# Performance work log

Measured on AMD Instinct MI355X. Metric: run time of the kernel, lower is better.

The kernel has to match this reference:

```python
import jax, jax.numpy as jnp
import numpy as np

D_MODEL = 1024
N_HEADS = 16
D_FF = 4096
EPS = 1e-6


def layernorm(x, alpha, bias):
    # torch.std uses Bessel correction (ddof=1)
    mean = jnp.mean(x, axis=-1, keepdims=True)
    std = jnp.std(x, axis=-1, keepdims=True, ddof=1)
    return alpha * (x - mean) / (std + EPS) + bias


def setup_inputs() -> dict:
    key = jax.random.key(0)
    ks = jax.random.split(key, 12)
    s = 1.0 / np.sqrt(D_MODEL)
    sf = 1.0 / np.sqrt(D_FF)
    return {
        "x": jax.random.normal(ks[0], (2, 2048, D_MODEL), jnp.float32),
        "mask": jnp.ones((2, 1, 1, 2048), jnp.int32),
        "wq": jax.random.normal(ks[1], (D_MODEL, D_MODEL), jnp.float32) * s,
        "wk": jax.random.normal(ks[2], (D_MODEL, D_MODEL), jnp.float32) * s,
        "wv": jax.random.normal(ks[3], (D_MODEL, D_MODEL), jnp.float32) * s,
        "wo": jax.random.normal(ks[4], (D_MODEL, D_MODEL), jnp.float32) * s,
        "wo_b": jnp.zeros((D_MODEL,), jnp.float32),
        "w1": jax.random.normal(ks[5], (D_MODEL, D_FF), jnp.float32) * s,
        "b1": jnp.zeros((D_FF,), jnp.float32),
        "w2": jax.random.normal(ks[6], (D_FF, D_MODEL), jnp.float32) * sf,
        "b2": jnp.zeros((D_MODEL,), jnp.float32),
        "alpha1": jnp.ones((D_MODEL,), jnp.float32),
        "bias1": jnp.zeros((D_MODEL,), jnp.float32),
        "alpha2": jnp.ones((D_MODEL,), jnp.float32),
        "bias2": jnp.zeros((D_MODEL,), jnp.float32),
    }


def reference(x, mask, wq, wk, wv, wo, wo_b, w1, b1, w2, b2,
              alpha1, bias1, alpha2, bias2):
    B, S, D = x.shape
    h, dk = N_HEADS, D_MODEL // N_HEADS
    # projections -> [B, h, S, dk]
    q = (x @ wq).reshape(B, S, h, dk).transpose(0, 2, 1, 3)
    k = (x @ wk).reshape(B, S, h, dk).transpose(0, 2, 1, 3)
    v = (x @ wv).reshape(B, S, h, dk).transpose(0, 2, 1, 3)
    scores = jnp.einsum('bhqd,bhkd->bhqk', q, k) / jnp.sqrt(jnp.float32(dk))
    scores = jnp.where(mask == 0, jnp.float32(-1e9), scores)
    attn = jax.nn.softmax(scores, axis=-1)
    ctx = jnp.einsum('bhqk,bhkd->bhqd', attn, v)
    ctx = ctx.transpose(0, 2, 1, 3).reshape(B, S, D)
    attn_out = ctx @ wo + wo_b
    x = layernorm(x + attn_out, alpha1, bias1)
    ff = jax.nn.relu(x @ w1 + b1) @ w2 + b2
    x = layernorm(x + ff, alpha2, bias2)
    return x
```

## Files before the change

### kernel.cpp

```cpp
#include <hip/hip_runtime.h>
#include <hip/hip_bf16.h>

#define D_MODEL 1024
#define N_HEADS 16
#define DK      64
#define SEQ     2048
#define BATCH   2
#define D_FF    4096
#define ROWS    (BATCH*SEQ)
#define LN_EPS  1e-6f
#define KTILE   128

typedef __hip_bfloat16 bf16;
typedef __attribute__((ext_vector_type(8))) short frag8;
typedef __attribute__((ext_vector_type(4))) float facc4;

__device__ inline float bf2f(unsigned short u){ return __uint_as_float(((unsigned)u) << 16); }
__device__ inline float toF(bf16 v){ return __bfloat162float(v); }
__device__ inline unsigned short f2bu(float f){ bf16 h = __float2bfloat16(f); return *reinterpret_cast<unsigned short*>(&h); }

__device__ inline unsigned cvtpk_bf16(float lo, float hi){
    unsigned r;
    asm("v_cvt_pk_bf16_f32 %0, %1, %2" : "=v"(r) : "v"(lo), "v"(hi));
    return r;
}

__device__ inline float ld1(const void* p, size_t idx, bool f32) {
    return f32 ? ((const float*)p)[idx] : toF(((const bf16*)p)[idx]);
}

struct U8 { unsigned short v[8]; };
__device__ inline U8 ld8bf(const void* p, size_t idx, bool f32) {
    U8 r;
    if (!f32) {
        *reinterpret_cast<uint4*>(r.v) = *reinterpret_cast<const uint4*>((const unsigned short*)p + idx);
    } else {
        const float* f = (const float*)p + idx;
        const float4 a = *reinterpret_cast<const float4*>(f);
        const float4 b = *reinterpret_cast<const float4*>(f + 4);
        r.v[0]=f2bu(a.x); r.v[1]=f2bu(a.y); r.v[2]=f2bu(a.z); r.v[3]=f2bu(a.w);
        r.v[4]=f2bu(b.x); r.v[5]=f2bu(b.y); r.v[6]=f2bu(b.z); r.v[7]=f2bu(b.w);
    }
    return r;
}

__device__ inline void gld16(const void* g, void* l) {
    __builtin_amdgcn_global_load_lds(
        reinterpret_cast<const __attribute__((address_space(1))) void*>(
            reinterpret_cast<uintptr_t>(g)),
        reinterpret_cast<__attribute__((address_space(3))) void*>(
            (unsigned int)reinterpret_cast<uintptr_t>(l)),
        16, 0, 0);
}

__global__ void probe_kernel(const void* __restrict__ xp, int* __restrict__ flag) {
    __shared__ int hit;
    if (threadIdx.x == 0) hit = 0;
    __syncthreads();
    const bf16* p = (const bf16*)xp;
    int bad = 0;
    for (int i = threadIdx.x; i < 8192; i += 256) {
        float v = fabsf(toF(p[i]));
        if (!(v <= 1e5f)) bad = 1;
    }
    if (bad) atomicOr(&hit, 1);
    __syncthreads();
    if (threadIdx.x == 0) *flag = hit;
}

__global__ __launch_bounds__(256) void xcvt_kernel(const void* __restrict__ x,
    bf16* __restrict__ out, const int* __restrict__ flagp)
{
    const bool f32 = (*flagp) != 0;
    const size_t i = ((size_t)blockIdx.x * 256 + threadIdx.x) * 8;
    U8 d = ld8bf(x, i, f32);
    *reinterpret_cast<uint4*>(out + i) = *reinterpret_cast<const uint4*>(d.v);
}

__global__ __launch_bounds__(256) void transpose_kernel(const void* __restrict__ W,
    bf16* __restrict__ WT, int K, int N, const int* __restrict__ flagp)
{
    const bool f32 = (*flagp) != 0;
    __shared__ float tile[64][65];
    const int t  = threadIdx.x;
    const int n0 = blockIdx.x * 64, k0 = blockIdx.y * 64;
    const int lr = t >> 2;
    const int lc = (t & 3) * 16;
    if (!f32) {
        const unsigned short* src = (const unsigned short*)W + (size_t)(k0 + lr) * N + n0 + lc;
        uint4 u0 = *reinterpret_cast<const uint4*>(src);
        uint4 u1 = *reinterpret_cast<const uint4*>(src + 8);
        const unsigned short* us0 = reinterpret_cast<const unsigned short*>(&u0);
        const unsigned short* us1 = reinterpret_cast<const unsigned short*>(&u1);
        #pragma unroll
        for (int j = 0; j < 8; ++j) {
            tile[lr][lc + j]     = bf2f(us0[j]);
            tile[lr][lc + 8 + j] = bf2f(us1[j]);
        }
    } else {
        const float* src = (const float*)W + (size_t)(k0 + lr) * N + n0 + lc;
        #pragma unroll
        for (int q4 = 0; q4 < 4; ++q4) {
            const float4 f = *reinterpret_cast<const float4*>(src + 4 * q4);
            tile[lr][lc + 4*q4 + 0] = f.x;
            tile[lr][lc + 4*q4 + 1] = f.y;
            tile[lr][lc + 4*q4 + 2] = f.z;
            tile[lr][lc + 4*q4 + 3] = f.w;
        }
    }
    __syncthreads();
    unsigned short o[16];
    #pragma unroll
    for (int j = 0; j < 16; ++j) o[j] = f2bu(tile[lc + j][lr]);
    bf16* dst = WT + (size_t)(n0 + lr) * K + k0 + lc;
    *reinterpret_cast<uint4*>(dst)     = *reinterpret_cast<const uint4*>(&o[0]);
    *reinterpret_cast<uint4*>(dst + 8) = *reinterpret_cast<const uint4*>(&o[8]);
}

__global__ __launch_bounds__(256) void transpose4_kernel(const void* __restrict__ w0,
    const void* __restrict__ w1, const void* __restrict__ w2, const void* __restrict__ w3,
    bf16* __restrict__ WT4, const int* __restrict__ flagp)
{
    const bool f32 = (*flagp) != 0;
    const int which = blockIdx.z;
    const void* W = (which == 0) ? w0 : (which == 1) ? w1 : (which == 2) ? w2 : w3;
    bf16* WT = WT4 + (size_t)which * D_MODEL * D_MODEL;
    __shared__ float tile[64][65];
    const int t  = threadIdx.x;
    const int n0 = blockIdx.x * 64, k0 = blockIdx.y * 64;
    const int lr = t >> 2;
    const int lc = (t & 3) * 16;
    if (!f32) {
        const unsigned short* src = (const unsigned short*)W + (size_t)(k0 + lr) * D_MODEL + n0 + lc;
        uint4 u0 = *reinterpret_cast<const uint4*>(src);
        uint4 u1 = *reinterpret_cast<const uint4*>(src + 8);
        const unsigned short* us0 = reinterpret_cast<const unsigned short*>(&u0);
        const unsigned short* us1 = reinterpret_cast<const unsigned short*>(&u1);
        #pragma unroll
        for (int j = 0; j < 8; ++j) {
            tile[lr][lc + j]     = bf2f(us0[j]);
            tile[lr][lc + 8 + j] = bf2f(us1[j]);
        }
    } else {
        const float* src = (const float*)W + (size_t)(k0 + lr) * D_MODEL + n0 + lc;
        #pragma unroll
        for (int q4 = 0; q4 < 4; ++q4) {
            const float4 f = *reinterpret_cast<const float4*>(src + 4 * q4);
            tile[lr][lc + 4*q4 + 0] = f.x;
            tile[lr][lc + 4*q4 + 1] = f.y;
            tile[lr][lc + 4*q4 + 2] = f.z;
            tile[lr][lc + 4*q4 + 3] = f.w;
        }
    }
    __syncthreads();
    unsigned short o[16];
    #pragma unroll
    for (int j = 0; j < 16; ++j) o[j] = f2bu(tile[lc + j][lr]);
    bf16* dst = WT + (size_t)(n0 + lr) * D_MODEL + k0 + lc;
    *reinterpret_cast<uint4*>(dst)     = *reinterpret_cast<const uint4*>(&o[0]);
    *reinterpret_cast<uint4*>(dst + 8) = *reinterpret_cast<const uint4*>(&o[8]);
}

__global__ __launch_bounds__(256) void vtrans_kernel(const bf16* __restrict__ V,
    bf16* __restrict__ VT)
{
    __shared__ unsigned short tile[32][33];
    const int tx = threadIdx.x, ty = threadIdx.y;
    const int s0 = blockIdx.x * 32, d0 = blockIdx.y * 32;
    const int bh = blockIdx.z, b = bh >> 4, h = bh & 15;
    #pragma unroll
    for (int r = 0; r < 4; ++r)
        tile[ty + 8*r][tx] = *reinterpret_cast<const unsigned short*>(
            V + ((size_t)(b * SEQ + s0 + ty + 8*r)) * D_MODEL + h * DK + d0 + tx);
    __syncthreads();
    #pragma unroll
    for (int r = 0; r < 4; ++r)
        *reinterpret_cast<unsigned short*>(
            VT + ((size_t)(bh * DK + d0 + ty + 8*r)) * SEQ + s0 + tx) = tile[tx][ty + 8*r];
}

template<bool RELU, bool BIAS, int NMAT, int SPLITK>
__global__ __launch_bounds__(256) void mgemm_kernel(const bf16* __restrict__ A,
    const bf16* __restrict__ BT, const void* __restrict__ bias,
    bf16* __restrict__ C, int M, int N, int K, const int* __restrict__ flagp)
{
    const bool inF32 = (*flagp) != 0;

    __shared__ unsigned short sA[128 * 64];
    __shared__ unsigned short sB[128 * 64];

    int which = 0, colb = blockIdx.x;
    if (NMAT > 1) { which = blockIdx.x >> 3; colb = blockIdx.x & 7; }
    const int kslice = (SPLITK > 1) ? blockIdx.z : 0;
    const int Kspan  = K / SPLITK;
    const int kbase  = kslice * Kspan;
    const bf16* Bp = BT + (size_t)which * N * K;
    bf16*       Cp = C  + (size_t)which * M * N + (size_t)kslice * M * N;

    const int row0 = blockIdx.y * 128;
    const int col0 = colb * 128;

    const int t    = threadIdx.x;
    const int wave = t >> 6;
    const int lane = t & 63;
    const int lm   = lane & 15;
    const int q    = lane >> 4;
    const int wm   = (wave & 1) * 64;
    const int wn   = (wave >> 1) * 64;

    facc4 acc[4][4];
    #pragma unroll
    for (int i = 0; i < 4; ++i)
        #pragma unroll
        for (int j = 0; j < 4; ++j)
            acc[i][j] = (facc4){0.f, 0.f, 0.f, 0.f};

    for (int k0 = kbase; k0 < kbase + Kspan; k0 += 64) {
        __syncthreads();
        #pragma unroll
        for (int j = 0; j < 4; ++j) {
            const int ch = (wave * 4 + j) * 64 + lane;
            const int r  = ch >> 3;
            const int cs = ch & 7;
            const int c  = cs ^ (r & 7);
            gld16(A  + (size_t)(row0 + r) * K + k0 + 8 * c, &sA[(wave * 4 + j) * 512]);
            gld16(Bp + (size_t)(col0 + r) * K + k0 + 8 * c, &sB[(wave * 4 + j) * 512]);
        }
        __syncthreads();

        #pragma unroll
        for (int kk = 0; kk < 64; kk += 32) {
            const int cr = (kk >> 3) + q;
            frag8 af[4], bfr[4];
            #pragma unroll
            for (int im = 0; im < 4; ++im) {
                const int m = wm + 16 * im + lm;
                af[im] = *reinterpret_cast<const frag8*>(&sA[m * 64 + ((cr ^ (m & 7)) << 3)]);
            }
            #pragma unroll
            for (int in = 0; in < 4; ++in) {
                const int n = wn + 16 * in + lm;
                bfr[in] = *reinterpret_cast<const frag8*>(&sB[n * 64 + ((cr ^ (n & 7)) << 3)]);
            }
            #pragma unroll
            for (int im = 0; im < 4; ++im)
                #pragma unroll
                for (int in = 0; in < 4; ++in)
                    acc[im][in] = __builtin_amdgcn_mfma_f32_16x16x32_bf16(af[im], bfr[in], acc[im][in], 0, 0, 0);
        }
    }

    #pragma unroll
    for (int in = 0; in < 4; ++in) {
        const int col = col0 + wn + 16*in + lm;
        float bv = 0.f;
        if (BIAS && kslice == 0) bv = ld1(bias, col, inF32);
        #pragma unroll
        for (int im = 0; im < 4; ++im) {
            #pragma unroll
            for (int r = 0; r < 4; ++r) {
                const int row = row0 + wm + 16*im + 4*q + r;
                float v = acc[im][in][r] + bv;
                if (RELU) v = fmaxf(v, 0.f);
                Cp[(size_t)row * N + col] = __float2bfloat16(v);
            }
        }
    }
}

__global__ __launch_bounds__(256, 2) void fattn_kernel(
    const bf16* __restrict__ Qg, const bf16* __restrict__ Kg,
    const bf16* __restrict__ VTg, const int* __restrict__ mask,
    bf16* __restrict__ ctx)
{
    __shared__ unsigned short sK[2][128 * 64];
    __shared__ unsigned short sV[2][64 * 128];
    __shared__ __align__(16) float madd[SEQ];

    const int t    = threadIdx.x;
    const int lin  = blockIdx.x + 16 * (blockIdx.y + 16 * blockIdx.z);
    const int rid  = (lin & 7) * 64 + (lin >> 3);
    const int qt   = rid & 15;
    const int h    = (rid >> 4) & 15;
    const int b    = rid >> 8;
    const int q0   = qt * 128;
    const int bh   = b * N_HEADS + h;
    const int wave = t >> 6;
    const int lane = t & 63;
    const int lm   = lane & 15;
    const int qd   = lane >> 4;
    const bool qo  = (qd & 1) != 0;

    const float SCL = 0.18033688011112042f;

    auto stage = [&](int bi, int kt) {
        const int k0 = kt * KTILE;
        #pragma unroll
        for (int j = 0; j < 4; ++j) {
            const int ch = (wave * 4 + j) * 64 + lane;
            const int rK = ch >> 3, cK = (ch & 7) ^ (rK & 7);
            gld16(Kg + ((size_t)(b * SEQ + k0 + rK)) * D_MODEL + h * DK + 8 * cK,
                  &sK[bi][(wave * 4 + j) * 512]);
            const int rV = ch >> 4, cV = (ch & 15) ^ (rV & 15);
            gld16(VTg + ((size_t)(bh * DK + rV)) * SEQ + k0 + 8 * cV,
                  &sV[bi][(wave * 4 + j) * 512]);
        }
    };

    stage(0, 0);
    #pragma unroll
    for (int i = 0; i < SEQ / 256; ++i) {
        const int idx = i * 256 + t;
        madd[idx] = (mask[b * SEQ + idx] == 0) ? -1.442695e9f : 0.f;
    }

    frag8 qf[2][2];
    #pragma unroll
    for (int s = 0; s < 2; ++s) {
        const bf16* qsrc = Qg + ((size_t)(b * SEQ + q0 + 32 * wave + 16 * s + lm)) * D_MODEL + h * DK;
        qf[s][0] = *reinterpret_cast<const frag8*>(qsrc + 8 * qd);
        qf[s][1] = *reinterpret_cast<const frag8*>(qsrc + 32 + 8 * qd);
    }

    facc4 accO[2][4];
    #pragma unroll
    for (int s = 0; s < 2; ++s)
        #pragma unroll
        for (int in = 0; in < 4; ++in) accO[s][in] = (facc4){0.f, 0.f, 0.f, 0.f};
    float m_r[2] = {-1e30f, -1e30f}, l_r[2] = {0.f, 0.f};

    for (int kt = 0; kt < SEQ / KTILE; ++kt) {
        const int cur = kt & 1;
        const int k0  = kt * KTILE;
        __syncthreads();
        if (kt + 1 < SEQ / KTILE) stage(cur ^ 1, kt + 1);

        facc4 accST[2][8];
        #pragma unroll
        for (int s = 0; s < 2; ++s)
            #pragma unroll
            for (int i = 0; i < 8; ++i) accST[s][i] = (facc4){0.f, 0.f, 0.f, 0.f};
        __builtin_amdgcn_s_setprio(1);
        #pragma unroll
        for (int i = 0; i < 8; ++i) {
            #pragma unroll
            for (int s2 = 0; s2 < 2; ++s2) {
                const int cr = 4 * s2 + qd;
                frag8 kf = *reinterpret_cast<const frag8*>(
                    &sK[cur][(16 * i + lm) * 64 + ((cr ^ (lm & 7)) << 3)]);
                accST[0][i] = __builtin_amdgcn_mfma_f32_16x16x32_bf16(kf, qf[0][s2], accST[0][i], 0, 0, 0);
                accST[1][i] = __builtin_amdgcn_mfma_f32_16x16x32_bf16(kf, qf[1][s2], accST[1][i], 0, 0, 0);
            }
        }
        __builtin_amdgcn_s_setprio(0);

        facc4 vmx[2];
        #pragma unroll
        for (int s = 0; s < 2; ++s) vmx[s] = (facc4){-1e30f, -1e30f, -1e30f, -1e30f};
        #pragma unroll
        for (int i = 0; i < 8; ++i) {
            const facc4 mv = *reinterpret_cast<const facc4*>(&madd[k0 + 16 * i + 4 * qd]);
            #pragma unroll
            for (int s = 0; s < 2; ++s) {
                #pragma unroll
                for (int r = 0; r < 4; ++r) {
                    accST[s][i][r] = fmaf(accST[s][i][r], SCL, mv[r]);
                    vmx[s][r] = fmaxf(vmx[s][r], accST[s][i][r]);
                }
            }
        }
        float mn[2], alpha[2] = {1.f, 1.f};
        bool resc[2];
        #pragma unroll
        for (int s = 0; s < 2; ++s) {
            const float mloc = fmaxf(fmaxf(vmx[s][0], vmx[s][1]), fmaxf(vmx[s][2], vmx[s][3]));
            const bool skip = __all(mloc - m_r[s] <= 11.54f) != 0;
            resc[s] = !skip;
            if (skip) {
                mn[s] = m_r[s];
            } else {
                float m0 = mloc;
                m0 = fmaxf(m0, __shfl_xor(m0, 16));
                m0 = fmaxf(m0, __shfl_xor(m0, 32));
                mn[s] = fmaxf(m_r[s], m0);
                alpha[s] = __builtin_amdgcn_exp2f(m_r[s] - mn[s]);
                m_r[s] = mn[s];
            }
        }

        unsigned up[2][8][2];
        facc4 ps4[2];
        #pragma unroll
        for (int s = 0; s < 2; ++s) ps4[s] = (facc4){0.f, 0.f, 0.f, 0.f};
        #pragma unroll
        for (int s = 0; s < 2; ++s) {
            #pragma unroll
            for (int i = 0; i < 8; ++i) {
                const float p0 = __builtin_amdgcn_exp2f(accST[s][i][0] - mn[s]);
                const float p1 = __builtin_amdgcn_exp2f(accST[s][i][1] - mn[s]);
                const float p2 = __builtin_amdgcn_exp2f(accST[s][i][2] - mn[s]);
                const float p3 = __builtin_amdgcn_exp2f(accST[s][i][3] - mn[s]);
                ps4[s][0] += p0; ps4[s][1] += p1; ps4[s][2] += p2; ps4[s][3] += p3;
                up[s][i][0] = cvtpk_bf16(p0, p1);
                up[s][i][1] = cvtpk_bf16(p2, p3);
            }
        }
        #pragma unroll
        for (int s = 0; s < 2; ++s) {
            float ps = (ps4[s][0] + ps4[s][1]) + (ps4[s][2] + ps4[s][3]);
            ps += __shfl_xor(ps, 16);
            ps += __shfl_xor(ps, 32);
            if (resc[s]) {
                l_r[s] = l_r[s] * alpha[s] + ps;
                #pragma unroll
                for (int in = 0; in < 4; ++in)
                    #pragma unroll
                    for (int r = 0; r < 4; ++r) accO[s][in][r] *= alpha[s];
            } else {
                l_r[s] += ps;
            }
        }

        __builtin_amdgcn_s_setprio(1);
        #pragma unroll
        for (int c = 0; c < 4; ++c) {
            union { frag8 f; unsigned u[4]; } pf0_, pf1_;
            #pragma unroll
            for (int s = 0; s < 2; ++s) {
                unsigned a0 = up[s][2*c][0],     a1 = up[s][2*c][1];
                unsigned b0 = up[s][2*c + 1][0], b1 = up[s][2*c + 1][1];
                asm("v_permlane32_swap_b32 %0, %1" : "+v"(a0), "+v"(b0));
                asm("v_permlane32_swap_b32 %0, %1" : "+v"(a1), "+v"(b1));
                const unsigned t0 = qo ? a0 : b0;
                const unsigned t1 = qo ? a1 : b1;
                const unsigned r0 = __shfl_xor(t0, 16);
                const unsigned r1 = __shfl_xor(t1, 16);
                unsigned u0 = qo ? r0 : a0;
                unsigned u1 = qo ? r1 : a1;
                unsigned u2 = qo ? b0 : r0;
                unsigned u3 = qo ? b1 : r1;
                if (s == 0) { pf0_.u[0]=u0; pf0_.u[1]=u1; pf0_.u[2]=u2; pf0_.u[3]=u3; }
                else        { pf1_.u[0]=u0; pf1_.u[1]=u1; pf1_.u[2]=u2; pf1_.u[3]=u3; }
            }
            #pragma unroll
            for (int in = 0; in < 4; ++in) {
                const int cr = 4 * c + qd;
                frag8 vf = *reinterpret_cast<const frag8*>(
                    &sV[cur][(16 * in + lm) * 128 + ((cr ^ lm) << 3)]);
                accO[0][in] = __builtin_amdgcn_mfma_f32_16x16x32_bf16(vf, pf0_.f, accO[0][in], 0, 0, 0);
                accO[1][in] = __builtin_amdgcn_mfma_f32_16x16x32_bf16(vf, pf1_.f, accO[1][in], 0, 0, 0);
            }
        }
        __builtin_amdgcn_s_setprio(0);
    }

    #pragma unroll
    for (int s = 0; s < 2; ++s) {
        const float invl = 1.f / l_r[s];
        bf16* crow = ctx + ((size_t)(b * SEQ + q0 + 32 * wave + 16 * s + lm)) * D_MODEL + h * DK;
        #pragma unroll
        for (int in = 0; in < 4; ++in) {
            union { uint2 v; unsigned u[2]; } ov;
            ov.u[0] = cvtpk_bf16(accO[s][in][0] * invl, accO[s][in][1] * invl);
            ov.u[1] = cvtpk_bf16(accO[s][in][2] * invl, accO[s][in][3] * invl);
            *reinterpret_cast<uint2*>(crow + 16 * in + 4 * qd) = ov.v;
        }
    }
}

template<bool BASE_WS, bool OUT_WS>
__global__ __launch_bounds__(128) void ln_kernel(const void* __restrict__ base,
    const bf16* __restrict__ addv, const bf16* __restrict__ addv2,
    const void* __restrict__ alpha, const void* __restrict__ bias,
    void* __restrict__ outp, const int* __restrict__ flagp)
{
    const bool inF32 = (*flagp) != 0;
    __shared__ float red[2];
    __shared__ float red2[2];
    const int row = blockIdx.x, t = threadIdx.x;
    const size_t off = (size_t)row * D_MODEL + t * 8;

    float v[8];
    {
        const U8 bz = ld8bf(base, off, BASE_WS ? false : inF32);
        uint4 a1 = *reinterpret_cast<const uint4*>(addv + off);
        const unsigned short* a1s = reinterpret_cast<const unsigned short*>(&a1);
        #pragma unroll
        for (int j = 0; j < 8; ++j) v[j] = bf2f(bz.v[j]) + bf2f(a1s[j]);
        if (addv2) {
            uint4 a2 = *reinterpret_cast<const uint4*>(addv2 + off);
            const unsigned short* a2s = reinterpret_cast<const unsigned short*>(&a2);
            #pragma unroll
            for (int j = 0; j < 8; ++j) v[j] += bf2f(a2s[j]);
        }
    }

    float s = ((v[0]+v[1]) + (v[2]+v[3])) + ((v[4]+v[5]) + (v[6]+v[7]));
    #pragma unroll
    for (int o = 1; o < 64; o <<= 1) s += __shfl_xor(s, o);
    if ((t & 63) == 0) red[t >> 6] = s;
    __syncthreads();
    const float mean = (red[0] + red[1]) * (1.f / (float)D_MODEL);

    float sq = 0.f;
    #pragma unroll
    for (int j = 0; j < 8; ++j) { const float d = v[j] - mean; sq += d * d; }
    #pragma unroll
    for (int o = 1; o < 64; o <<= 1) sq += __shfl_xor(sq, o);
    if ((t & 63) == 0) red2[t >> 6] = sq;
    __syncthreads();
    const float var = (red2[0] + red2[1]) * (1.f / (float)(D_MODEL - 1));
    const float inv = 1.f / (sqrtf(var) + LN_EPS);

    float y[8];
    #pragma unroll
    for (int j = 0; j < 8; ++j)
        y[j] = ld1(alpha, t * 8 + j, inF32) * (v[j] - mean) * inv + ld1(bias, t * 8 + j, inF32);

    if (OUT_WS || !inF32) {
        union { uint4 u; unsigned w[4]; } o_;
        o_.w[0] = cvtpk_bf16(y[0], y[1]);
        o_.w[1] = cvtpk_bf16(y[2], y[3]);
        o_.w[2] = cvtpk_bf16(y[4], y[5]);
        o_.w[3] = cvtpk_bf16(y[6], y[7]);
        *reinterpret_cast<uint4*>((bf16*)outp + off) = o_.u;
    } else {
        float* op = (float*)outp + off;
        const float4 f0 = {y[0], y[1], y[2], y[3]};
        const float4 f1 = {y[4], y[5], y[6], y[7]};
        *reinterpret_cast<float4*>(op)     = f0;
        *reinterpret_cast<float4*>(op + 4) = f1;
    }
}

extern "C" void kernel_launch(void* const* d_in, const int* in_sizes, int n_in,
                              void* d_out, int out_size, void* d_ws, size_t ws_size,
                              hipStream_t stream)
{
    const void* x    = d_in[0];
    const int*  mask = (const int*)d_in[1];
    const void* wq   = d_in[2];
    const void* wk   = d_in[3];
    const void* wv   = d_in[4];
    const void* wo   = d_in[5];
    const void* wo_b = d_in[6];
    const void* w1   = d_in[7];
    const void* b1   = d_in[8];
    const void* w2   = d_in[9];
    const void* b2   = d_in[10];
    const void* al1  = d_in[11];
    const void* bi1  = d_in[12];
    const void* al2  = d_in[13];
    const void* bi2  = d_in[14];

    const size_t MB = 1024 * 1024;
    char* ws = (char*)d_ws;
    const bool BIG = ws_size >= 64 * MB + 4096;
    if (!BIG && ws_size < 56 * MB + 4096) return;

    dim3 tb(32, 8);

    if (BIG) {
        bf16* Qb   = (bf16*)(ws + 0 * MB);
        bf16* Kb   = (bf16*)(ws + 8 * MB);
        bf16* Vb   = (bf16*)(ws + 16 * MB);
        bf16* Xb   = (bf16*)(ws + 24 * MB);
        bf16* VTb  = (bf16*)(ws + 24 * MB);
        bf16* WT4  = (bf16*)(ws + 32 * MB);
        bf16* WOT  = WT4 + (size_t)3 * D_MODEL * D_MODEL;
        bf16* W1T  = (bf16*)(ws + 40 * MB);
        bf16* W2T  = (bf16*)(ws + 48 * MB);
        bf16* CTXb = (bf16*)(ws + 56 * MB);
        bf16* ATT0 = (bf16*)(ws + 0 * MB);
        bf16* ATT1 = (bf16*)(ws + 8 * MB);
        bf16* X1b  = (bf16*)(ws + 56 * MB);
        bf16* FFb  = (bf16*)(ws + 0 * MB);
        bf16* X20  = (bf16*)(ws + 32 * MB);
        bf16* X21  = (bf16*)(ws + 40 * MB);
        int*  flagp = (int*)(ws + 64 * MB);

        probe_kernel<<<1, 256, 0, stream>>>(x, flagp);
        xcvt_kernel<<<dim3(ROWS * D_MODEL / 2048), 256, 0, stream>>>(x, Xb, flagp);

        transpose4_kernel<<<dim3(16, 16, 4), 256, 0, stream>>>(wq, wk, wv, wo, WT4, flagp);
        transpose_kernel<<<dim3(64, 16), 256, 0, stream>>>(w1, W1T, D_MODEL, D_FF, flagp);
        transpose_kernel<<<dim3(16, 64), 256, 0, stream>>>(w2, W2T, D_FF, D_MODEL, flagp);

        mgemm_kernel<false, false, 3, 1><<<dim3(24, 32), 256, 0, stream>>>(
            Xb, WT4, nullptr, Qb, ROWS, D_MODEL, D_MODEL, flagp);

        vtrans_kernel<<<dim3(SEQ / 32, 2, BATCH * N_HEADS), tb, 0, stream>>>(Vb, VTb);

        fattn_kernel<<<dim3(SEQ / 128, N_HEADS, BATCH), 256, 0, stream>>>(Qb, Kb, VTb, mask, CTXb);

        mgemm_kernel<false, true, 1, 2><<<dim3(8, 32, 2), 256, 0, stream>>>(
            CTXb, WOT, wo_b, ATT0, ROWS, D_MODEL, D_MODEL, flagp);
        ln_kernel<false, true><<<ROWS, 128, 0, stream>>>(x, ATT0, ATT1, al1, bi1, X1b, flagp);

        mgemm_kernel<true, true, 1, 1><<<dim3(32, 32), 256, 0, stream>>>(
            X1b, W1T, b1, FFb, ROWS, D_FF, D_MODEL, flagp);

        mgemm_kernel<false, true, 1, 2><<<dim3(8, 32, 2), 256, 0, stream>>>(
            FFb, W2T, b2, X20, ROWS, D_MODEL, D_FF, flagp);
        ln_kernel<true, false><<<ROWS, 128, 0, stream>>>(X1b, X20, X21, al2, bi2, d_out, flagp);
    } else {
        bf16* Qb    = (bf16*)(ws + 0 * MB);
        bf16* Kb    = (bf16*)(ws + 8 * MB);
        bf16* Vb    = (bf16*)(ws + 16 * MB);
        bf16* Xb    = (bf16*)(ws + 24 * MB);
        bf16* VTb   = (bf16*)(ws + 24 * MB);
        bf16* WQKVT = (bf16*)(ws + 32 * MB);
        bf16* CTXb  = (bf16*)(ws + 32 * MB);
        bf16* W2T   = (bf16*)(ws + 32 * MB);
        bf16* WOT   = (bf16*)(ws + 0 * MB);
        bf16* ATT0  = (bf16*)(ws + 48 * MB);
        bf16* W1T   = (bf16*)(ws + 48 * MB);
        bf16* X20   = (bf16*)(ws + 48 * MB);
        bf16* X1b   = (bf16*)(ws + 40 * MB);
        bf16* FFb   = (bf16*)(ws + 0 * MB);
        int*  flagp = (int*)(ws + 56 * MB);

        probe_kernel<<<1, 256, 0, stream>>>(x, flagp);
        xcvt_kernel<<<dim3(ROWS * D_MODEL / 2048), 256, 0, stream>>>(x, Xb, flagp);

        transpose_kernel<<<dim3(16, 16), 256, 0, stream>>>(wq, WQKVT,           D_MODEL, D_MODEL, flagp);
        transpose_kernel<<<dim3(16, 16), 256, 0, stream>>>(wk, WQKVT + 1048576, D_MODEL, D_MODEL, flagp);
        transpose_kernel<<<dim3(16, 16), 256, 0, stream>>>(wv, WQKVT + 2097152, D_MODEL, D_MODEL, flagp);

        mgemm_kernel<false, false, 3, 1><<<dim3(24, 32), 256, 0, stream>>>(
            Xb, WQKVT, nullptr, Qb, ROWS, D_MODEL, D_MODEL, flagp);

        vtrans_kernel<<<dim3(SEQ / 32, 2, BATCH * N_HEADS), tb, 0, stream>>>(Vb, VTb);

        fattn_kernel<<<dim3(SEQ / 128, N_HEADS, BATCH), 256, 0, stream>>>(Qb, Kb, VTb, mask, CTXb);

        transpose_kernel<<<dim3(16, 16), 256, 0, stream>>>(wo, WOT, D_MODEL, D_MODEL, flagp);
        mgemm_kernel<false, true, 1, 1><<<dim3(8, 32), 256, 0, stream>>>(
            CTXb, WOT, wo_b, ATT0, ROWS, D_MODEL, D_MODEL, flagp);
        ln_kernel<false, true><<<ROWS, 128, 0, stream>>>(x, ATT0, nullptr, al1, bi1, X1b, flagp);

        transpose_kernel<<<dim3(64, 16), 256, 0, stream>>>(w1, W1T, D_MODEL, D_FF, flagp);
        mgemm_kernel<true, true, 1, 1><<<dim3(32, 32), 256, 0, stream>>>(
            X1b, W1T, b1, FFb, ROWS, D_FF, D_MODEL, flagp);

        transpose_kernel<<<dim3(16, 64), 256, 0, stream>>>(w2, W2T, D_FF, D_MODEL, flagp);
        mgemm_kernel<false, true, 1, 1><<<dim3(8, 32), 256, 0, stream>>>(
            FFb, W2T, b2, X20, ROWS, D_MODEL, D_FF, flagp);
        ln_kernel<true, false><<<ROWS, 128, 0, stream>>>(X1b, X20, nullptr, al2, bi2, d_out, flagp);
    }
}
```

Measured before the change: 381.4 us.

## Fuse V transpose into QKV GEMM epilogue and merge FF weight transposes

The QKV GEMM now writes the V projection directly in per-head transposed layout [b,h,d,s], which removes the separate vtrans kernel and its extra read and write of V. The two FFN weight transposes are merged into one launch. The attention mask is loaded as int4 vectors, and layernorm loads alpha and bias as 8-wide vectors. The transposed V epilogue uses strided 8-byte stores that may coalesce less well than the normal row-major epilogue.

```diff
diff --git a/kernel.cpp b/kernel.cpp
--- a/kernel.cpp
+++ b/kernel.cpp
@@ -44,6 +44,21 @@
     return r;
 }
 
+__device__ inline void ld8f(const void* p, int idx, bool f32, float* o) {
+    if (!f32) {
+        uint4 u = *reinterpret_cast<const uint4*>((const unsigned short*)p + idx);
+        const unsigned short* us = reinterpret_cast<const unsigned short*>(&u);
+        #pragma unroll
+        for (int j = 0; j < 8; ++j) o[j] = bf2f(us[j]);
+    } else {
+        const float* f = (const float*)p + idx;
+        const float4 a = *reinterpret_cast<const float4*>(f);
+        const float4 b = *reinterpret_cast<const float4*>(f + 4);
+        o[0]=a.x; o[1]=a.y; o[2]=a.z; o[3]=a.w;
+        o[4]=b.x; o[5]=b.y; o[6]=b.z; o[7]=b.w;
+    }
+}
+
 __device__ inline void gld16(const void* g, void* l) {
     __builtin_amdgcn_global_load_lds(
         reinterpret_cast<const __attribute__((address_space(1))) void*>(
@@ -77,13 +92,9 @@
     *reinterpret_cast<uint4*>(out + i) = *reinterpret_cast<const uint4*>(d.v);
 }
 
-__global__ __launch_bounds__(256) void transpose_kernel(const void* __restrict__ W,
-    bf16* __restrict__ WT, int K, int N, const int* __restrict__ flagp)
-{
-    const bool f32 = (*flagp) != 0;
-    __shared__ float tile[64][65];
-    const int t  = threadIdx.x;
-    const int n0 = blockIdx.x * 64, k0 = blockIdx.y * 64;
+__device__ inline void ttile(const void* W, bf16* WT, int K, int N,
+                             int n0, int k0, bool f32, float (*tile)[65], int t)
+{
     const int lr = t >> 2;
     const int lc = (t & 3) * 16;
     if (!f32) {
@@ -117,66 +128,37 @@
     *reinterpret_cast<uint4*>(dst + 8) = *reinterpret_cast<const uint4*>(&o[8]);
 }
 
+__global__ __launch_bounds__(256) void transpose_kernel(const void* __restrict__ W,
+    bf16* __restrict__ WT, int K, int N, const int* __restrict__ flagp)
+{
+    __shared__ float tile[64][65];
+    ttile(W, WT, K, N, blockIdx.x * 64, blockIdx.y * 64, (*flagp) != 0, tile, threadIdx.x);
+}
+
 __global__ __launch_bounds__(256) void transpose4_kernel(const void* __restrict__ w0,
     const void* __restrict__ w1, const void* __restrict__ w2, const void* __restrict__ w3,
     bf16* __restrict__ WT4, const int* __restrict__ flagp)
 {
-    const bool f32 = (*flagp) != 0;
     const int which = blockIdx.z;
     const void* W = (which == 0) ? w0 : (which == 1) ? w1 : (which == 2) ? w2 : w3;
     bf16* WT = WT4 + (size_t)which * D_MODEL * D_MODEL;
     __shared__ float tile[64][65];
-    const int t  = threadIdx.x;
-    const int n0 = blockIdx.x * 64, k0 = blockIdx.y * 64;
-    const int lr = t >> 2;
-    const int lc = (t & 3) * 16;
-    if (!f32) {
-        const unsigned short* src = (const unsigned short*)W + (size_t)(k0 + lr) * D_MODEL + n0 + lc;
-        uint4 u0 = *reinterpret_cast<const uint4*>(src);
-        uint4 u1 = *reinterpret_cast<const uint4*>(src + 8);
-        const unsigned short* us0 = reinterpret_cast<const unsigned short*>(&u0);
-        const unsigned short* us1 = reinterpret_cast<const unsigned short*>(&u1);
-        #pragma unroll
-        for (int j = 0; j < 8; ++j) {
-            tile[lr][lc + j]     = bf2f(us0[j]);
-            tile[lr][lc + 8 + j] = bf2f(us1[j]);
-        }
-    } else {
-        const float* src = (const float*)W + (size_t)(k0 + lr) * D_MODEL + n0 + lc;
-        #pragma unroll
-        for (int q4 = 0; q4 < 4; ++q4) {
-            const float4 f = *reinterpret_cast<const float4*>(src + 4 * q4);
-            tile[lr][lc + 4*q4 + 0] = f.x;
-            tile[lr][lc + 4*q4 + 1] = f.y;
-            tile[lr][lc + 4*q4 + 2] = f.z;
-            tile[lr][lc + 4*q4 + 3] = f.w;
-        }
-    }
-    __syncthreads();
-    unsigned short o[16];
-    #pragma unroll
-    for (int j = 0; j < 16; ++j) o[j] = f2bu(tile[lc + j][lr]);
-    bf16* dst = WT + (size_t)(n0 + lr) * D_MODEL + k0 + lc;
-    *reinterpret_cast<uint4*>(dst)     = *reinterpret_cast<const uint4*>(&o[0]);
-    *reinterpret_cast<uint4*>(dst + 8) = *reinterpret_cast<const uint4*>(&o[8]);
-}
-
-__global__ __launch_bounds__(256) void vtrans_kernel(const bf16* __restrict__ V,
-    bf16* __restrict__ VT)
-{
-    __shared__ unsigned short tile[32][33];
-    const int tx = threadIdx.x, ty = threadIdx.y;
-    const int s0 = blockIdx.x * 32, d0 = blockIdx.y * 32;
-    const int bh = blockIdx.z, b = bh >> 4, h = bh & 15;
-    #pragma unroll
-    for (int r = 0; r < 4; ++r)
-        tile[ty + 8*r][tx] = *reinterpret_cast<const unsigned short*>(
-            V + ((size_t)(b * SEQ + s0 + ty + 8*r)) * D_MODEL + h * DK + d0 + tx);
-    __syncthreads();
-    #pragma unroll
-    for (int r = 0; r < 4; ++r)
-        *reinterpret_cast<unsigned short*>(
-            VT + ((size_t)(bh * DK + d0 + ty + 8*r)) * SEQ + s0 + tx) = tile[tx][ty + 8*r];
+    ttile(W, WT, D_MODEL, D_MODEL, blockIdx.x * 64, blockIdx.y * 64, (*flagp) != 0, tile, threadIdx.x);
+}
+
+__global__ __launch_bounds__(256) void transposeFF_kernel(const void* __restrict__ w1,
+    const void* __restrict__ w2, bf16* __restrict__ W1T, bf16* __restrict__ W2T,
+    const int* __restrict__ flagp)
+{
+    __shared__ float tile[64][65];
+    const int z = blockIdx.y, bid = blockIdx.x;
+    const void* W = z ? w2 : w1;
+    bf16* WT = z ? W2T : W1T;
+    const int K = z ? D_FF : D_MODEL;
+    const int N = z ? D_MODEL : D_FF;
+    const int n0 = (z ? (bid & 15) : (bid & 63)) * 64;
+    const int k0 = (z ? (bid >> 4) : (bid >> 6)) * 64;
+    ttile(W, WT, K, N, n0, k0, (*flagp) != 0, tile, threadIdx.x);
 }
 
 template<bool RELU, bool BIAS, int NMAT, int SPLITK>
@@ -248,6 +230,24 @@
                 for (int in = 0; in < 4; ++in)
                     acc[im][in] = __builtin_amdgcn_mfma_f32_16x16x32_bf16(af[im], bfr[in], acc[im][in], 0, 0, 0);
         }
+    }
+
+    if (NMAT > 1 && which == 2) {
+        #pragma unroll
+        for (int in = 0; in < 4; ++in) {
+            const int col = col0 + wn + 16*in + lm;
+            const int hh = col >> 6, dd = col & 63;
+            #pragma unroll
+            for (int im = 0; im < 4; ++im) {
+                const int rowb = row0 + wm + 16*im + 4*q;
+                const int bb = rowb >> 11, ss = rowb & 2047;
+                union { uint2 v; unsigned u[2]; } ov;
+                ov.u[0] = cvtpk_bf16(acc[im][in][0], acc[im][in][1]);
+                ov.u[1] = cvtpk_bf16(acc[im][in][2], acc[im][in][3]);
+                *reinterpret_cast<uint2*>(Cp + ((size_t)((bb * 16 + hh) * 64 + dd)) * 2048 + ss) = ov.v;
+            }
+        }
+        return;
     }
 
     #pragma unroll
@@ -309,9 +309,13 @@
 
     stage(0, 0);
     #pragma unroll
-    for (int i = 0; i < SEQ / 256; ++i) {
-        const int idx = i * 256 + t;
-        madd[idx] = (mask[b * SEQ + idx] == 0) ? -1.442695e9f : 0.f;
+    for (int i = 0; i < SEQ / (256 * 4); ++i) {
+        const int idx = (i * 256 + t) * 4;
+        const int4 mv = *reinterpret_cast<const int4*>(&mask[b * SEQ + idx]);
+        madd[idx + 0] = (mv.x == 0) ? -1.442695e9f : 0.f;
+        madd[idx + 1] = (mv.y == 0) ? -1.442695e9f : 0.f;
+        madd[idx + 2] = (mv.z == 0) ? -1.442695e9f : 0.f;
+        madd[idx + 3] = (mv.w == 0) ? -1.442695e9f : 0.f;
     }
 
     frag8 qf[2][2];
@@ -512,10 +516,13 @@
     const float var = (red2[0] + red2[1]) * (1.f / (float)(D_MODEL - 1));
     const float inv = 1.f / (sqrtf(var) + LN_EPS);
 
+    float av[8], bv[8];
+    ld8f(alpha, t * 8, inF32, av);
+    ld8f(bias,  t * 8, inF32, bv);
     float y[8];
     #pragma unroll
     for (int j = 0; j < 8; ++j)
-        y[j] = ld1(alpha, t * 8 + j, inF32) * (v[j] - mean) * inv + ld1(bias, t * 8 + j, inF32);
+        y[j] = av[j] * (v[j] - mean) * inv + bv[j];
 
     if (OUT_WS || !inF32) {
         union { uint4 u; unsigned w[4]; } o_;
@@ -558,14 +565,11 @@
     const bool BIG = ws_size >= 64 * MB + 4096;
     if (!BIG && ws_size < 56 * MB + 4096) return;
 
-    dim3 tb(32, 8);
-
     if (BIG) {
         bf16* Qb   = (bf16*)(ws + 0 * MB);
+        bf16* VTb  = (bf16*)(ws + 16 * MB);
+        bf16* Xb   = (bf16*)(ws + 24 * MB);
         bf16* Kb   = (bf16*)(ws + 8 * MB);
-        bf16* Vb   = (bf16*)(ws + 16 * MB);
-        bf16* Xb   = (bf16*)(ws + 24 * MB);
-        bf16* VTb  = (bf16*)(ws + 24 * MB);
         bf16* WT4  = (bf16*)(ws + 32 * MB);
         bf16* WOT  = WT4 + (size_t)3 * D_MODEL * D_MODEL;
         bf16* W1T  = (bf16*)(ws + 40 * MB);
@@ -583,13 +587,10 @@
         xcvt_kernel<<<dim3(ROWS * D_MODEL / 2048), 256, 0, stream>>>(x, Xb, flagp);
 
         transpose4_kernel<<<dim3(16, 16, 4), 256, 0, stream>>>(wq, wk, wv, wo, WT4, flagp);
-        transpose_kernel<<<dim3(64, 16), 256, 0, stream>>>(w1, W1T, D_MODEL, D_FF, flagp);
-        transpose_kernel<<<dim3(16, 64), 256, 0, stream>>>(w2, W2T, D_FF, D_MODEL, flagp);
+        transposeFF_kernel<<<dim3(1024, 2), 256, 0, stream>>>(w1, w2, W1T, W2T, flagp);
 
         mgemm_kernel<false, false, 3, 1><<<dim3(24, 32), 256, 0, stream>>>(
             Xb, WT4, nullptr, Qb, ROWS, D_MODEL, D_MODEL, flagp);
-
-        vtrans_kernel<<<dim3(SEQ / 32, 2, BATCH * N_HEADS), tb, 0, stream>>>(Vb, VTb);
 
         fattn_kernel<<<dim3(SEQ / 128, N_HEADS, BATCH), 256, 0, stream>>>(Qb, Kb, VTb, mask, CTXb);
 
@@ -606,9 +607,8 @@
     } else {
         bf16* Qb    = (bf16*)(ws + 0 * MB);
         bf16* Kb    = (bf16*)(ws + 8 * MB);
-        bf16* Vb    = (bf16*)(ws + 16 * MB);
+        bf16* VTb   = (bf16*)(ws + 16 * MB);
         bf16* Xb    = (bf16*)(ws + 24 * MB);
-        bf16* VTb   = (bf16*)(ws + 24 * MB);
         bf16* WQKVT = (bf16*)(ws + 32 * MB);
         bf16* CTXb  = (bf16*)(ws + 32 * MB);
         bf16* W2T   = (bf16*)(ws + 32 * MB);
@@ -630,8 +630,6 @@
         mgemm_kernel<false, false, 3, 1><<<dim3(24, 32), 256, 0, stream>>>(
             Xb, WQKVT, nullptr, Qb, ROWS, D_MODEL, D_MODEL, flagp);
 
-        vtrans_kernel<<<dim3(SEQ / 32, 2, BATCH * N_HEADS), tb, 0, stream>>>(Vb, VTb);
-
         fattn_kernel<<<dim3(SEQ / 128, N_HEADS, BATCH), 256, 0, stream>>>(Qb, Kb, VTb, mask, CTXb);
 
         transpose_kernel<<<dim3(16, 16), 256, 0, stream>>>(wo, WOT, D_MODEL, D_MODEL, flagp);
```

Measured after the change: 360.9 us. 5.4% less time.
